# Performance work log

Hardware: AMD Instinct MI355X
Metric: run time of the kernel (lower is better)

The kernel has to match this reference:

```python
import jax, jax.numpy as jnp
import numpy as np

N = 50000
E = 800000
IN = 128
HID = 32
OUT = 32
H1, H2 = 4, 4
NEG_SLOPE = 0.2


def setup_inputs() -> dict:
    key = jax.random.key(0)
    ks = jax.random.split(key, 12)
    x = jax.random.normal(ks[0], (N, IN), dtype=jnp.float32)
    src = jax.random.randint(ks[1], (E,), 0, N, dtype=jnp.int32)
    dst = jax.random.randint(ks[2], (E,), 0, N, dtype=jnp.int32)
    s = 0.1
    # layer 1: fc (IN -> H1*HID, no bias), attn vectors (H1, HID), bias (H1*HID,)
    W1 = jax.random.normal(ks[3], (IN, H1 * HID), dtype=jnp.float32) * s
    al1 = jax.random.normal(ks[4], (H1, HID), dtype=jnp.float32) * s
    ar1 = jax.random.normal(ks[5], (H1, HID), dtype=jnp.float32) * s
    b1 = jnp.zeros((H1 * HID,), dtype=jnp.float32)
    # layer 2: fc (H1*HID -> H2*OUT, no bias)
    W2 = jax.random.normal(ks[6], (H1 * HID, H2 * OUT), dtype=jnp.float32) * s
    al2 = jax.random.normal(ks[7], (H2, OUT), dtype=jnp.float32) * s
    ar2 = jax.random.normal(ks[8], (H2, OUT), dtype=jnp.float32) * s
    b2 = jnp.zeros((H2 * OUT,), dtype=jnp.float32)
    return {"x": x, "W1": W1, "al1": al1, "ar1": ar1, "b1": b1,
            "W2": W2, "al2": al2, "ar2": ar2, "b2": b2,
            "src": src, "dst": dst}


def _gat_layer(x, W, al, ar, b, src, dst, n, h, d):
    # feat_drop is identity (eval mode)
    feat = (x @ W).reshape(n, h, d)                       # [N,H,D]
    el = jnp.einsum('nhd,hd->nh', feat, al)               # [N,H]
    er = jnp.einsum('nhd,hd->nh', feat, ar)               # [N,H]
    e = jax.nn.leaky_relu(el[src] + er[dst], NEG_SLOPE)   # [E,H] SDDMM
    # edge softmax over incoming edges of each destination node
    emax = jax.ops.segment_max(e, dst, num_segments=n)    # [N,H]
    emax = jnp.where(jnp.isfinite(emax), emax, 0.0)       # guard 0-in-degree
    w = jnp.exp(e - emax[dst])                            # [E,H]
    denom = jax.ops.segment_sum(w, dst, num_segments=n)   # [N,H]
    alpha = w / jnp.maximum(denom[dst], 1e-9)             # [E,H]; attn_drop identity
    # SpMM aggregation
    rst = jax.ops.segment_sum(feat[src] * alpha[:, :, None], dst, num_segments=n)
    # residual: in_feats == h*d for both layers -> DGL uses Identity res_fc
    rst = rst + x.reshape(n, h, d)
    rst = rst + b.reshape(1, h, d)
    return rst


def reference(x, W1, al1, ar1, b1, W2, al2, ar2, b2, src, dst):
    h = _gat_layer(x, W1, al1, ar1, b1, src, dst, N, H1, HID)
    h = jax.nn.elu(h)                                     # layer-1 activation
    h = h.reshape(N, H1 * HID)                            # flatten(1)
    h = _gat_layer(h, W2, al2, ar2, b2, src, dst, N, H2, OUT)
    return h.mean(axis=1)                                 # [N,OUT]
```

## Files before the change

kernel.cpp:

```cpp
#include <hip/hip_runtime.h>
#include <cstdint>
#include <cstddef>

#define NEG_SLOPE 0.2f

typedef __bf16 bf16x8 __attribute__((ext_vector_type(8)));
typedef float  f32x4  __attribute__((ext_vector_type(4)));

__device__ inline unsigned int bf16pair(float a, float b) {
    unsigned int ua = __float_as_uint(a), ub = __float_as_uint(b);
    ua += 0x7fffu + ((ua >> 16) & 1u);
    ub += 0x7fffu + ((ub >> 16) & 1u);
    return (ua >> 16) | (ub & 0xffff0000u);
}
__device__ inline unsigned short bf16r(float x) {
    unsigned int u = __float_as_uint(x);
    u += 0x7fffu + ((u >> 16) & 1u);
    return (unsigned short)(u >> 16);
}

__global__ __launch_bounds__(256) void wtrans_kernel(
    const float* __restrict__ W1, const float* __restrict__ W2,
    unsigned short* __restrict__ Wt1, unsigned short* __restrict__ Wt2)
{
    __shared__ float tile[64][65];
    const float* W = (blockIdx.x < 4) ? W1 : W2;
    unsigned short* Wt = (blockIdx.x < 4) ? Wt1 : Wt2;
    const int tb = blockIdx.x & 3;
    const int k0 = (tb >> 1) * 64, n0 = (tb & 1) * 64;
    const int c = threadIdx.x & 63, r4 = threadIdx.x >> 6;
#pragma unroll
    for (int i = 0; i < 16; ++i) {
        const int r = i * 4 + r4;
        tile[r][c] = W[(size_t)(k0 + r) * 128 + n0 + c];
    }
    __syncthreads();
#pragma unroll
    for (int i = 0; i < 16; ++i) {
        const int nn = i * 4 + r4;
        Wt[(size_t)(n0 + nn) * 128 + k0 + c] = bf16r(tile[c][nn]);
    }
}

__global__ __launch_bounds__(256, 3) void gemm_attn_kernel(
    const float* __restrict__ X, const unsigned short* __restrict__ Wt,
    const float* __restrict__ al, const float* __restrict__ ar,
    unsigned short* __restrict__ feat16, float* __restrict__ el,
    float* __restrict__ er, int n)
{
    __shared__ unsigned short sX[64][136];
    __shared__ unsigned short sW[128][136];

    const int t = threadIdx.x;
    const int rowbase = blockIdx.x * 64;

#pragma unroll
    for (int i = 0; i < 8; ++i) {
        const int idx = t + 256 * i;
        const int row = idx >> 5;
        const int kq  = (idx & 31) * 4;
        int g = rowbase + row; if (g >= n) g = n - 1;
        const float4 v = *(const float4*)&X[(size_t)g * 128 + kq];
        uint2 pk;
        pk.x = bf16pair(v.x, v.y);
        pk.y = bf16pair(v.z, v.w);
        *(uint2*)&sX[row][kq] = pk;
    }
#pragma unroll
    for (int i = 0; i < 8; ++i) {
        const int idx = t + 256 * i;
        const int row = idx >> 4;
        const int q   = idx & 15;
        *(uint4*)&sW[row][q * 8] = *(const uint4*)&Wt[(size_t)row * 128 + q * 8];
    }
    __syncthreads();

    const int lane = t & 63;
    const int w    = t >> 6;
    const int m    = lane & 15;
    const int g4   = lane >> 4;

    bf16x8 a[4];
#pragma unroll
    for (int ks = 0; ks < 4; ++ks)
        a[ks] = *(const bf16x8*)&sX[w * 16 + m][ks * 32 + g4 * 8];

    float elacc[4][4] = {{0}}, eracc[4][4] = {{0}};

#pragma unroll
    for (int ct = 0; ct < 8; ct += 2) {
        f32x4 acc0 = {0.f, 0.f, 0.f, 0.f}, acc1 = {0.f, 0.f, 0.f, 0.f};
        const int n0 = ct * 16 + m, n1 = n0 + 16;
#pragma unroll
        for (int ks = 0; ks < 4; ++ks) {
            const bf16x8 b0 = *(const bf16x8*)&sW[n0][ks * 32 + g4 * 8];
            const bf16x8 b1 = *(const bf16x8*)&sW[n1][ks * 32 + g4 * 8];
            acc0 = __builtin_amdgcn_mfma_f32_16x16x32_bf16(a[ks], b0, acc0, 0, 0, 0);
            acc1 = __builtin_amdgcn_mfma_f32_16x16x32_bf16(a[ks], b1, acc1, 0, 0, 0);
        }
        const int h = ct >> 1;
        const float al0 = al[n0], ar0 = ar[n0];
        const float al1 = al[n1], ar1 = ar[n1];
#pragma unroll
        for (int r = 0; r < 4; ++r) {
            elacc[r][h] += acc0[r] * al0 + acc1[r] * al1;
            eracc[r][h] += acc0[r] * ar0 + acc1[r] * ar1;
            const int row = rowbase + w * 16 + g4 * 4 + r;
            if (row < n) {
                feat16[(size_t)row * 128 + n0] = bf16r(acc0[r]);
                feat16[(size_t)row * 128 + n1] = bf16r(acc1[r]);
            }
        }
    }

#pragma unroll
    for (int r = 0; r < 4; ++r)
#pragma unroll
        for (int h = 0; h < 4; ++h) {
            float a_ = elacc[r][h], b_ = eracc[r][h];
            a_ += __shfl_xor(a_, 1); b_ += __shfl_xor(b_, 1);
            a_ += __shfl_xor(a_, 2); b_ += __shfl_xor(b_, 2);
            a_ += __shfl_xor(a_, 4); b_ += __shfl_xor(b_, 4);
            a_ += __shfl_xor(a_, 8); b_ += __shfl_xor(b_, 8);
            elacc[r][h] = a_; eracc[r][h] = b_;
        }
    if (m == 0) {
#pragma unroll
        for (int r = 0; r < 4; ++r) {
            const int row = rowbase + w * 16 + g4 * 4 + r;
            if (row < n) {
#pragma unroll
                for (int h = 0; h < 4; ++h) {
                    el[(size_t)row * 4 + h] = elacc[r][h];
                    er[(size_t)row * 4 + h] = eracc[r][h];
                }
            }
        }
    }
}

__global__ void degree_kernel(const int* __restrict__ dst, int* __restrict__ deg, int E)
{
    const int e4 = (blockIdx.x * blockDim.x + threadIdx.x) * 4;
    if (e4 + 4 <= E) {
        const int4 d = *(const int4*)&dst[e4];
        atomicAdd(&deg[d.x], 1);
        atomicAdd(&deg[d.y], 1);
        atomicAdd(&deg[d.z], 1);
        atomicAdd(&deg[d.w], 1);
    } else {
        for (int e = e4; e < E; ++e) atomicAdd(&deg[dst[e]], 1);
    }
}

__global__ __launch_bounds__(1024) void scan_kernel(
    const int* __restrict__ deg, int* __restrict__ off, int n)
{
    __shared__ int wsums[16];
    __shared__ int s_carry;
    const int tid  = threadIdx.x;
    const int lane = tid & 63;
    const int wid  = tid >> 6;

    if (tid == 0) { s_carry = 0; off[0] = 0; }
    __syncthreads();

    const int n4 = n >> 2;
    const int4* __restrict__ deg4 = (const int4*)deg;

    for (int base = 0; base < n4; base += 1024) {
        const int i4 = base + tid;
        int4 v = make_int4(0, 0, 0, 0);
        if (i4 < n4) v = deg4[i4];
        const int t0 = v.x, t1 = t0 + v.y, t2 = t1 + v.z, t3 = t2 + v.w;

        int x = t3;
#pragma unroll
        for (int d = 1; d < 64; d <<= 1) {
            int y = __shfl_up(x, d);
            if (lane >= d) x += y;
        }
        if (lane == 63) wsums[wid] = x;
        __syncthreads();

        if (wid == 0 && lane < 16) {
            int xx = wsums[lane];
#pragma unroll
            for (int d = 1; d < 16; d <<= 1) {
                int y = __shfl_up(xx, d);
                if (lane >= d) xx += y;
            }
            wsums[lane] = xx;
        }
        __syncthreads();

        const int wp   = (wid == 0) ? 0 : wsums[wid - 1];
        const int excl = s_carry + wp + (x - t3);
        if (i4 < n4) {
            off[4 * i4 + 1] = excl + t0;
            off[4 * i4 + 2] = excl + t1;
            off[4 * i4 + 3] = excl + t2;
            off[4 * i4 + 4] = excl + t3;
        }
        __syncthreads();
        if (tid == 0) s_carry += wsums[15];
        __syncthreads();
    }
}

__global__ void scatter_kernel(const int* __restrict__ src, const int* __restrict__ dst,
                               const int* __restrict__ off, int* __restrict__ cursor,
                               int* __restrict__ csr_src, int E)
{
    const int e4 = (blockIdx.x * blockDim.x + threadIdx.x) * 4;
    if (e4 + 4 <= E) {
        const int4 s = *(const int4*)&src[e4];
        const int4 d = *(const int4*)&dst[e4];
        const int o0 = off[d.x], o1 = off[d.y], o2 = off[d.z], o3 = off[d.w];
        const int p0 = atomicAdd(&cursor[d.x], 1);
        const int p1 = atomicAdd(&cursor[d.y], 1);
        const int p2 = atomicAdd(&cursor[d.z], 1);
        const int p3 = atomicAdd(&cursor[d.w], 1);
        csr_src[o0 + p0] = s.x;
        csr_src[o1 + p1] = s.y;
        csr_src[o2 + p2] = s.z;
        csr_src[o3 + p3] = s.w;
    } else {
        for (int e = e4; e < E; ++e) {
            const int d = dst[e];
            const int pos = off[d] + atomicAdd(&cursor[d], 1);
            csr_src[pos] = src[e];
        }
    }
}

template <bool LAYER2>
__global__ __launch_bounds__(256) void agg_kernel(
    const int* __restrict__ off, const int* __restrict__ csr_src,
    const unsigned short* __restrict__ feat16, const float* __restrict__ el,
    const float* __restrict__ er, const float* __restrict__ resid,
    const float* __restrict__ bias, float* __restrict__ out, int n)
{
    const int lane = threadIdx.x & 63;
    const int node = blockIdx.x * 4 + (threadIdx.x >> 6);
    if (node >= n) return;

    const int h  = lane >> 4;
    const int d0 = 2 * lane;

    const float erh = er[(size_t)node * 4 + h];
    const unsigned int* __restrict__ fb = (const unsigned int*)feat16;

    const int beg = off[node], end = off[node + 1];

    float acc0 = 0.f, acc1 = 0.f, sw = 0.f;
    int j = beg;

#define EDGE4(J)                                                              \
    {                                                                         \
        const int s0 = csr_src[J], s1 = csr_src[(J) + 1];                     \
        const int s2 = csr_src[(J) + 2], s3 = csr_src[(J) + 3];               \
        const float e0 = el[(size_t)s0 * 4 + h];                              \
        const float e1 = el[(size_t)s1 * 4 + h];                              \
        const float e2 = el[(size_t)s2 * 4 + h];                              \
        const float e3 = el[(size_t)s3 * 4 + h];                              \
        const unsigned int u0 = fb[(size_t)s0 * 64 + lane];                   \
        const unsigned int u1 = fb[(size_t)s1 * 64 + lane];                   \
        const unsigned int u2 = fb[(size_t)s2 * 64 + lane];                   \
        const unsigned int u3 = fb[(size_t)s3 * 64 + lane];                   \
        float a0 = e0 + erh, a1 = e1 + erh, a2 = e2 + erh, a3 = e3 + erh;     \
        a0 = (a0 >= 0.f) ? a0 : NEG_SLOPE * a0;                               \
        a1 = (a1 >= 0.f) ? a1 : NEG_SLOPE * a1;                               \
        a2 = (a2 >= 0.f) ? a2 : NEG_SLOPE * a2;                               \
        a3 = (a3 >= 0.f) ? a3 : NEG_SLOPE * a3;                               \
        const float w0 = __expf(a0), w1 = __expf(a1);                         \
        const float w2 = __expf(a2), w3 = __expf(a3);                         \
        acc0 += w0 * __uint_as_float(u0 << 16);                               \
        acc1 += w0 * __uint_as_float(u0 & 0xffff0000u);                       \
        acc0 += w1 * __uint_as_float(u1 << 16);                               \
        acc1 += w1 * __uint_as_float(u1 & 0xffff0000u);                       \
        acc0 += w2 * __uint_as_float(u2 << 16);                               \
        acc1 += w2 * __uint_as_float(u2 & 0xffff0000u);                       \
        acc0 += w3 * __uint_as_float(u3 << 16);                               \
        acc1 += w3 * __uint_as_float(u3 & 0xffff0000u);                       \
        sw += w0 + w1 + w2 + w3;                                              \
    }

    for (; j + 8 <= end; j += 8) { EDGE4(j) EDGE4(j + 4) }
    for (; j + 4 <= end; j += 4) { EDGE4(j) }
#undef EDGE4
    for (; j < end; ++j) {
        const int s = csr_src[j];
        float e = el[(size_t)s * 4 + h] + erh;
        e = (e >= 0.f) ? e : NEG_SLOPE * e;
        const float w = __expf(e);
        const unsigned int u = fb[(size_t)s * 64 + lane];
        acc0 += w * __uint_as_float(u << 16);
        acc1 += w * __uint_as_float(u & 0xffff0000u);
        sw += w;
    }

    const float inv = 1.f / fmaxf(sw, 1e-9f);
    const float2 rs = *(const float2*)&resid[(size_t)node * 128 + d0];
    float v0 = acc0 * inv + rs.x + bias[d0];
    float v1 = acc1 * inv + rs.y + bias[d0 + 1];

    if (!LAYER2) {
        v0 = (v0 > 0.f) ? v0 : expm1f(v0);
        v1 = (v1 > 0.f) ? v1 : expm1f(v1);
        *(float2*)&out[(size_t)node * 128 + d0] = make_float2(v0, v1);
    } else {
        float s0 = v0, s1 = v1;
        s0 += __shfl_xor(s0, 16); s1 += __shfl_xor(s1, 16);
        s0 += __shfl_xor(s0, 32); s1 += __shfl_xor(s1, 32);
        if (lane < 16)
            *(float2*)&out[(size_t)node * 32 + 2 * lane] =
                make_float2(s0 * 0.25f, s1 * 0.25f);
    }
}

extern "C" void kernel_launch(void* const* d_in, const int* in_sizes, int n_in,
                              void* d_out, int out_size, void* d_ws, size_t ws_size,
                              hipStream_t stream)
{
    const float* x   = (const float*)d_in[0];
    const float* W1  = (const float*)d_in[1];
    const float* al1 = (const float*)d_in[2];
    const float* ar1 = (const float*)d_in[3];
    const float* b1  = (const float*)d_in[4];
    const float* W2  = (const float*)d_in[5];
    const float* al2 = (const float*)d_in[6];
    const float* ar2 = (const float*)d_in[7];
    const float* b2  = (const float*)d_in[8];
    const int*   src = (const int*)d_in[9];
    const int*   dst = (const int*)d_in[10];

    const int n = in_sizes[0] / 128;
    const int E = in_sizes[9];
    float* out = (float*)d_out;

    char* p = (char*)d_ws;
    float* h1    = (float*)p;          p += (size_t)n * 128 * sizeof(float);
    unsigned short* feat16 = (unsigned short*)p; p += (size_t)n * 128 * sizeof(unsigned short);
    float* el    = (float*)p;          p += (size_t)n * 4 * sizeof(float);
    float* er    = (float*)p;          p += (size_t)n * 4 * sizeof(float);
    int* off     = (int*)p;            p += (size_t)(n + 1) * sizeof(int);
    int* deg     = (int*)p;            p += (size_t)n * sizeof(int);
    int* cursor  = (int*)p;            p += (size_t)n * sizeof(int);
    int* csr     = (int*)p;            p += (size_t)E * sizeof(int);
    unsigned short* wt1 = (unsigned short*)p; p += (size_t)128 * 128 * sizeof(unsigned short);
    unsigned short* wt2 = (unsigned short*)p; p += (size_t)128 * 128 * sizeof(unsigned short);

    hipMemsetAsync(deg, 0, (size_t)(2 * n) * sizeof(int), stream);

    const int gemm_grid  = (n + 63) / 64;
    const int edge4_grid = (E / 4 + 255) / 256;
    const int agg_grid   = (n + 3) / 4;

    wtrans_kernel<<<8, 256, 0, stream>>>(W1, W2, wt1, wt2);
    gemm_attn_kernel<<<gemm_grid, 256, 0, stream>>>(x, wt1, al1, ar1, feat16, el, er, n);
    degree_kernel<<<edge4_grid, 256, 0, stream>>>(dst, deg, E);
    scan_kernel<<<1, 1024, 0, stream>>>(deg, off, n);
    scatter_kernel<<<edge4_grid, 256, 0, stream>>>(src, dst, off, cursor, csr, E);
    agg_kernel<false><<<agg_grid, 256, 0, stream>>>(off, csr, feat16, el, er, x, b1, h1, n);
    gemm_attn_kernel<<<gemm_grid, 256, 0, stream>>>(h1, wt2, al2, ar2, feat16, el, er, n);
    agg_kernel<true><<<agg_grid, 256, 0, stream>>>(off, csr, feat16, el, er, h1, b2, out, n);
}
```

Baseline: 301.3 us.

## Stage GEMM bf16 output through LDS and record edge ranks in degree pass

The GEMM epilogue now buffers the bf16 feature tile in registers, writes it to shared memory, and stores it back with coalesced 16-byte row writes instead of scattered 2-byte stores. The degree kernel also saves each edge's atomic return value as its rank within its destination, so the placement pass needs no second round of atomics and no cursor array. This trades one extra E-sized int array write and read plus two block barriers for fewer uncoalesced stores and half the atomics.

```diff
diff --git a/kernel.cpp b/kernel.cpp
--- a/kernel.cpp
+++ b/kernel.cpp
@@ -86,6 +86,7 @@
         a[ks] = *(const bf16x8*)&sX[w * 16 + m][ks * 32 + g4 * 8];
 
     float elacc[4][4] = {{0}}, eracc[4][4] = {{0}};
+    unsigned short fout[8][4];
 
 #pragma unroll
     for (int ct = 0; ct < 8; ct += 2) {
@@ -105,10 +106,27 @@
         for (int r = 0; r < 4; ++r) {
             elacc[r][h] += acc0[r] * al0 + acc1[r] * al1;
             eracc[r][h] += acc0[r] * ar0 + acc1[r] * ar1;
-            const int row = rowbase + w * 16 + g4 * 4 + r;
-            if (row < n) {
-                feat16[(size_t)row * 128 + n0] = bf16r(acc0[r]);
-                feat16[(size_t)row * 128 + n1] = bf16r(acc1[r]);
+            fout[ct][r]     = bf16r(acc0[r]);
+            fout[ct + 1][r] = bf16r(acc1[r]);
+        }
+    }
+
+    __syncthreads();
+#pragma unroll
+    for (int ct = 0; ct < 8; ++ct)
+#pragma unroll
+        for (int r = 0; r < 4; ++r)
+            sX[w * 16 + g4 * 4 + r][(ct & 1) * 16 + (ct >> 1) * 32 + m] = fout[ct][r];
+    __syncthreads();
+    {
+        const int row = t >> 2;
+        const int q   = t & 3;
+        const int g   = rowbase + row;
+        if (g < n) {
+#pragma unroll
+            for (int i = 0; i < 4; ++i) {
+                const int c0 = q * 8 + i * 32;
+                *(uint4*)&feat16[(size_t)g * 128 + c0] = *(const uint4*)&sX[row][c0];
             }
         }
     }
@@ -139,17 +157,21 @@
     }
 }
 
-__global__ void degree_kernel(const int* __restrict__ dst, int* __restrict__ deg, int E)
+
+__global__ void rank_kernel(const int* __restrict__ dst, int* __restrict__ deg,
+                            int* __restrict__ rank, int E)
 {
     const int e4 = (blockIdx.x * blockDim.x + threadIdx.x) * 4;
     if (e4 + 4 <= E) {
         const int4 d = *(const int4*)&dst[e4];
-        atomicAdd(&deg[d.x], 1);
-        atomicAdd(&deg[d.y], 1);
-        atomicAdd(&deg[d.z], 1);
-        atomicAdd(&deg[d.w], 1);
+        int4 r;
+        r.x = atomicAdd(&deg[d.x], 1);
+        r.y = atomicAdd(&deg[d.y], 1);
+        r.z = atomicAdd(&deg[d.z], 1);
+        r.w = atomicAdd(&deg[d.w], 1);
+        *(int4*)&rank[e4] = r;
     } else {
-        for (int e = e4; e < E; ++e) atomicAdd(&deg[dst[e]], 1);
+        for (int e = e4; e < E; ++e) rank[e] = atomicAdd(&deg[dst[e]], 1);
     }
 }
 
@@ -208,29 +230,23 @@
     }
 }
 
-__global__ void scatter_kernel(const int* __restrict__ src, const int* __restrict__ dst,
-                               const int* __restrict__ off, int* __restrict__ cursor,
-                               int* __restrict__ csr_src, int E)
+__global__ void place_kernel(const int* __restrict__ src, const int* __restrict__ dst,
+                             const int* __restrict__ off, const int* __restrict__ rank,
+                             int* __restrict__ csr_src, int E)
 {
     const int e4 = (blockIdx.x * blockDim.x + threadIdx.x) * 4;
     if (e4 + 4 <= E) {
         const int4 s = *(const int4*)&src[e4];
         const int4 d = *(const int4*)&dst[e4];
+        const int4 r = *(const int4*)&rank[e4];
         const int o0 = off[d.x], o1 = off[d.y], o2 = off[d.z], o3 = off[d.w];
-        const int p0 = atomicAdd(&cursor[d.x], 1);
-        const int p1 = atomicAdd(&cursor[d.y], 1);
-        const int p2 = atomicAdd(&cursor[d.z], 1);
-        const int p3 = atomicAdd(&cursor[d.w], 1);
-        csr_src[o0 + p0] = s.x;
-        csr_src[o1 + p1] = s.y;
-        csr_src[o2 + p2] = s.z;
-        csr_src[o3 + p3] = s.w;
+        csr_src[o0 + r.x] = s.x;
+        csr_src[o1 + r.y] = s.y;
+        csr_src[o2 + r.z] = s.z;
+        csr_src[o3 + r.w] = s.w;
     } else {
-        for (int e = e4; e < E; ++e) {
-            const int d = dst[e];
-            const int pos = off[d] + atomicAdd(&cursor[d], 1);
-            csr_src[pos] = src[e];
-        }
+        for (int e = e4; e < E; ++e)
+            csr_src[off[dst[e]] + rank[e]] = src[e];
     }
 }
 
@@ -346,12 +362,12 @@
     float* er    = (float*)p;          p += (size_t)n * 4 * sizeof(float);
     int* off     = (int*)p;            p += (size_t)(n + 1) * sizeof(int);
     int* deg     = (int*)p;            p += (size_t)n * sizeof(int);
-    int* cursor  = (int*)p;            p += (size_t)n * sizeof(int);
+    int* rank    = (int*)p;            p += (size_t)E * sizeof(int);
     int* csr     = (int*)p;            p += (size_t)E * sizeof(int);
     unsigned short* wt1 = (unsigned short*)p; p += (size_t)128 * 128 * sizeof(unsigned short);
     unsigned short* wt2 = (unsigned short*)p; p += (size_t)128 * 128 * sizeof(unsigned short);
 
-    hipMemsetAsync(deg, 0, (size_t)(2 * n) * sizeof(int), stream);
+    hipMemsetAsync(deg, 0, (size_t)n * sizeof(int), stream);
 
     const int gemm_grid  = (n + 63) / 64;
     const int edge4_grid = (E / 4 + 255) / 256;
@@ -359,9 +375,9 @@
 
     wtrans_kernel<<<8, 256, 0, stream>>>(W1, W2, wt1, wt2);
     gemm_attn_kernel<<<gemm_grid, 256, 0, stream>>>(x, wt1, al1, ar1, feat16, el, er, n);
-    degree_kernel<<<edge4_grid, 256, 0, stream>>>(dst, deg, E);
+    rank_kernel<<<edge4_grid, 256, 0, stream>>>(dst, deg, rank, E);
     scan_kernel<<<1, 1024, 0, stream>>>(deg, off, n);
-    scatter_kernel<<<edge4_grid, 256, 0, stream>>>(src, dst, off, cursor, csr, E);
+    place_kernel<<<edge4_grid, 256, 0, stream>>>(src, dst, off, rank, csr, E);
     agg_kernel<false><<<agg_grid, 256, 0, stream>>>(off, csr, feat16, el, er, x, b1, h1, n);
     gemm_attn_kernel<<<gemm_grid, 256, 0, stream>>>(h1, wt2, al2, ar2, feat16, el, er, n);
     agg_kernel<true><<<agg_grid, 256, 0, stream>>>(off, csr, feat16, el, er, h1, b2, out, n);
```

Measured after the change: 270.1 us. 10.4% less time.
